# Kernel optimization log

Hardware: AMD Instinct MI355X
Metric: run time of the kernel (lower is better)

## Reference

```python
import jax, jax.numpy as jnp
import numpy as np
import math

IN_F, OUT_F = 4096, 4096
ORDER, TENSOR_RANK = 4, 8
LEAF_A = math.ceil(IN_F ** (1.0 / ORDER))   # 8
LEAF_B = math.ceil(OUT_F ** (1.0 / ORDER))  # 8


def setup_inputs() -> dict:
    key = jax.random.key(0)
    k1, k2, k3, k4 = jax.random.split(key, 4)
    x = jax.random.normal(k1, (8, 2048, IN_F), dtype=jnp.float32)
    weight = jax.random.normal(k2, (OUT_F, IN_F), dtype=jnp.float32) * 0.02
    bias = jax.random.normal(k3, (OUT_F,), dtype=jnp.float32) * 0.02
    # reset_parameters: gain for leaky_relu(sqrt(5)) = sqrt(2/(1+5)); std = gain / in_features**(1/order)
    gain = math.sqrt(2.0 / (1.0 + 5.0))
    std = gain / (IN_F ** (1.0 / ORDER))
    weight_leafs = jax.random.uniform(
        k4, (ORDER, TENSOR_RANK, LEAF_A, LEAF_B), dtype=jnp.float32,
        minval=-std, maxval=std)
    return {"x": x, "weight": weight, "bias": bias, "weight_leafs": weight_leafs}


def _reproduce_weight(weight_leafs):
    # Original einsum 'lij,rmn->rimjn' sums the FIRST operand over its leading
    # (rank) axis; chained through both stages + final .sum(0), every leaf is
    # summed over tensor_rank. Exact math = nested Kronecker of the rank-summed
    # leaves, sliced to [:in_features, :out_features].
    s = weight_leafs.sum(axis=1)  # (4, a, b)
    a, b = LEAF_A, LEAF_B
    z1 = jnp.einsum('ij,mn->imjn', s[0], s[1]).reshape(a * a, b * b)
    z2 = jnp.einsum('ij,mn->imjn', s[2], s[3]).reshape(a * a, b * b)
    zzz = jnp.einsum('ij,mn->imjn', z1, z2).reshape(a ** 4, b ** 4)
    return zzz[:IN_F, :OUT_F]  # (in_features, out_features)


def reference(x, weight, bias, weight_leafs):
    tensor_weight = _reproduce_weight(weight_leafs)       # (in, out)
    full_weight = weight + tensor_weight.T                # (out, in)
    # F.linear: x @ W^T + b
    return jnp.einsum('bsi,oi->bso', x, full_weight) + bias
```

## Files before the change

kernel.cpp:

```cpp
#include <hip/hip_runtime.h>
#include <hip/hip_bf16.h>
#include <stdint.h>

typedef __attribute__((ext_vector_type(8))) __bf16 bf16x8;
typedef __attribute__((ext_vector_type(4))) float f32x4;

#define IN_F   4096
#define OUT_F  4096
#define M_ROWS 16384

static __device__ __forceinline__ unsigned short f2bf(float f) {
    unsigned int u = __float_as_uint(f);
    u += 0x7FFFu + ((u >> 16) & 1u);
    return (unsigned short)(u >> 16);
}

#define PREP_WBLK 1366
#define PREP_NBLK 4096

__global__ __launch_bounds__(256) void prep_kernel(
    const float* __restrict__ weight, const float* __restrict__ leafs,
    const float* __restrict__ x,
    unsigned short* __restrict__ wb, unsigned short* __restrict__ xbuf)
{
    const int t = threadIdx.x;
    if (blockIdx.x < PREP_WBLK) {
        __shared__ float s[4][8][8];
        {
            const int o = t >> 6, a = (t >> 3) & 7, b = t & 7;
            float acc = 0.f;
            #pragma unroll
            for (int r = 0; r < 8; ++r)
                acc += leafs[o * 512 + r * 64 + a * 8 + b];
            s[o][a][b] = acc;
        }
        __syncthreads();

        const int total = (OUT_F * IN_F) / 8;
        for (int idx = blockIdx.x * 256 + t; idx < total; idx += PREP_WBLK * 256) {
            const int n  = idx >> 9;
            const int kg = idx & 511;
            const int n0 = n >> 9, n1 = (n >> 6) & 7, n2 = (n >> 3) & 7, n3 = n & 7;
            const int k0 = kg >> 6, k1 = (kg >> 3) & 7, k2 = kg & 7;
            const float p = s[0][k0][n0] * s[1][k1][n1] * s[2][k2][n2];
            const float4* wp = (const float4*)(weight + (size_t)n * IN_F + kg * 8);
            const float4 w0 = wp[0], w1 = wp[1];
            const float wv[8] = {w0.x, w0.y, w0.z, w0.w, w1.x, w1.y, w1.z, w1.w};
            unsigned int pk[4];
            #pragma unroll
            for (int j = 0; j < 4; ++j) {
                unsigned int lo = f2bf(wv[2*j]   + p * s[3][2*j]  [n3]);
                unsigned int hi = f2bf(wv[2*j+1] + p * s[3][2*j+1][n3]);
                pk[j] = lo | (hi << 16);
            }
            *reinterpret_cast<uint4*>(wb + (size_t)n * IN_F + kg * 8) =
                make_uint4(pk[0], pk[1], pk[2], pk[3]);
        }
    } else {
        const long long n8 = (long long)M_ROWS * IN_F / 8;
        const int xblocks = PREP_NBLK - PREP_WBLK;
        for (long long idx = (long long)(blockIdx.x - PREP_WBLK) * 256 + t;
             idx < n8; idx += (long long)xblocks * 256) {
            const float4* xp = (const float4*)(x + idx * 8);
            const float4 a = xp[0], b = xp[1];
            const float v[8] = {a.x, a.y, a.z, a.w, b.x, b.y, b.z, b.w};
            unsigned int pk[4];
            #pragma unroll
            for (int j = 0; j < 4; ++j)
                pk[j] = (unsigned int)f2bf(v[2*j]) | ((unsigned int)f2bf(v[2*j+1]) << 16);
            *reinterpret_cast<uint4*>(xbuf + idx * 8) =
                make_uint4(pk[0], pk[1], pk[2], pk[3]);
        }
    }
}

#define BK 64
#define NT 64

#define PANEL_A(b,kk) (ldsb + ((b)*2+(kk))*16384)
#define PANEL_B(b,kk) (ldsb + 65536 + ((b)*2+(kk))*16384)

#define GLL(src, dst) __builtin_amdgcn_global_load_lds( \
    (const __attribute__((address_space(1))) void*)(src), \
    (__attribute__((address_space(3))) void*)(dst), 16, 0, 0)

#define STAGE_A(b, kk, ko) do { \
    GLL(sA1 + (ko) + (kk)*32,          PANEL_A(b,kk) + d1); \
    GLL(sA1 + 524288 + (ko) + (kk)*32, PANEL_A(b,kk) + d1 + 8192); } while(0)
#define STAGE_B(b, kk, ko) do { \
    GLL(sB1 + (ko) + (kk)*32,          PANEL_B(b,kk) + d1); \
    GLL(sB1 + 524288 + (ko) + (kk)*32, PANEL_B(b,kk) + d1 + 8192); } while(0)

#define SB0  __builtin_amdgcn_sched_barrier(0)
#define BAR  __builtin_amdgcn_s_barrier()
#define PRI1 __builtin_amdgcn_s_setprio(1)
#define PRI0 __builtin_amdgcn_s_setprio(0)
#define WLG4 asm volatile("s_waitcnt lgkmcnt(4)" ::: "memory")
#define WLG0 asm volatile("s_waitcnt lgkmcnt(0)" ::: "memory")
#define WVM4 asm volatile("s_waitcnt vmcnt(4)" ::: "memory")
#define WVM0 asm volatile("s_waitcnt vmcnt(0)" ::: "memory")

#define HALF(P, KK, KO, PF) do { \
    if (PF) { STAGE_A((P)^1, KK, KO); STAGE_B((P)^1, KK, KO); } \
    _Pragma("unroll") \
    for (int i_ = 0; i_ < 4; ++i_) \
        aG1[i_] = *(const bf16x8*)(aB + (P)*32768 + (KK)*16384 + i_*1024); \
    _Pragma("unroll") \
    for (int i_ = 0; i_ < 4; ++i_) \
        bG[i_]  = *(const bf16x8*)(bB + (P)*32768 + (KK)*16384 + i_*1024); \
    _Pragma("unroll") \
    for (int i_ = 0; i_ < 4; ++i_) \
        aG2[i_] = *(const bf16x8*)(aB + (P)*32768 + (KK)*16384 + (4+i_)*1024); \
    SB0; WLG4; SB0; \
    PRI1; \
    _Pragma("unroll") \
    for (int m_ = 0; m_ < 4; ++m_) { _Pragma("unroll") \
    for (int n_ = 0; n_ < 4; ++n_) \
        acc[m_][n_] = __builtin_amdgcn_mfma_f32_16x16x32_bf16( \
            aG1[m_], bG[n_], acc[m_][n_], 0, 0, 0); } \
    PRI0; SB0; WLG0; SB0; \
    PRI1; \
    _Pragma("unroll") \
    for (int m_ = 0; m_ < 4; ++m_) { _Pragma("unroll") \
    for (int n_ = 0; n_ < 4; ++n_) \
        acc[4+m_][n_] = __builtin_amdgcn_mfma_f32_16x16x32_bf16( \
            aG2[m_], bG[n_], acc[4+m_][n_], 0, 0, 0); } \
    PRI0; SB0; \
    if (PF) { WVM4; } else { WVM0; } \
    BAR; SB0; \
} while (0)

__global__ __launch_bounds__(512, 2) void gemm2b_kernel(
    const unsigned short* __restrict__ xb,
    const unsigned short* __restrict__ wb,
    const float* __restrict__ bias,
    float* __restrict__ out)
{
    __shared__ unsigned short lds_us[65536];
    char* const ldsb = (char*)lds_us;

    const int t    = threadIdx.x;
    const int wave = t >> 6;
    const int lane = t & 63;
    const int lr   = lane & 15;
    const int kq   = lane >> 4;
    const int wr   = wave >> 2;
    const int wcn  = wave & 3;
    const int sx   = (lr & 6) << 3;

    const int bid  = blockIdx.x;
    const int swzb = (bid & 7) * 128 + (bid >> 3);
    const int bm   = (swzb >> 4) * 256;
    const int bn   = (swzb & 15) * 256;

    const int c1 = t;
    const int r1 = c1 >> 2;
    const int q1 = ((c1 & 3) * 16) ^ ((r1 & 6) << 3);
    const unsigned short* sA1 = xb + (size_t)(bm + r1) * IN_F + (q1 >> 1);
    const unsigned short* sB1 = wb + (size_t)(bn + r1) * IN_F + (q1 >> 1);
    const int d1 = c1 * 16;

    const char* aB = ldsb + (wr * 128 + lr) * 64 + ((kq * 16) ^ sx);
    const char* bB = ldsb + 65536 + (wcn * 64 + lr) * 64 + ((kq * 16) ^ sx);

    f32x4 acc[8][4] = {};
    bf16x8 aG1[4], aG2[4], bG[4];

    STAGE_A(0, 0, 0); STAGE_B(0, 0, 0); STAGE_A(0, 1, 0); STAGE_B(0, 1, 0);
    WVM4; BAR; SB0;

    #pragma unroll 1
    for (int tt = 0; tt < NT - 1; ++tt) {
        const int p  = tt & 1;
        const int ko = (tt + 1) * BK;
        HALF(p, 0, ko, true);
        HALF(p, 1, ko, true);
    }
    HALF(1, 0, 0, false);
    HALF(1, 1, 0, false);

    #pragma unroll
    for (int n = 0; n < 4; ++n) {
        const int col = bn + wcn * 64 + n * 16 + lr;
        const float bv = bias[col];
        #pragma unroll
        for (int m = 0; m < 8; ++m) {
            const size_t rb = (size_t)(bm + wr * 128 + m * 16 + kq * 4) * OUT_F + col;
            #pragma unroll
            for (int j = 0; j < 4; ++j)
                out[rb + (size_t)j * OUT_F] = acc[m][n][j] + bv;
        }
    }
}

#define FBM 128
#define FBN 128
#define FBK 32

__global__ __launch_bounds__(256) void gemm_fb_kernel(
    const float* __restrict__ xf,
    const unsigned short* __restrict__ wb,
    const float* __restrict__ bias,
    float* __restrict__ out)
{
    __shared__ unsigned short As[FBM * FBK];
    __shared__ unsigned short Bs[FBN * FBK];

    const int t    = threadIdx.x;
    const int wave = t >> 6;
    const int lane = t & 63;
    const int lr   = lane & 15;
    const int kq   = lane >> 4;
    const int wr   = wave >> 1;
    const int wc   = wave & 1;

    const int bm = blockIdx.x * FBM;
    const int bn = blockIdx.y * FBN;
    const int srow = t >> 2;
    const int scol = (t & 3) * 8;

    f32x4 acc[4][4] = {};

    for (int kt = 0; kt < IN_F; kt += FBK) {
        #pragma unroll
        for (int g = 0; g < 2; ++g) {
            const int row = srow + g * 64;
            const float4* xp = (const float4*)(xf + (size_t)(bm + row) * IN_F + kt + scol);
            const float4 a0 = xp[0], a1 = xp[1];
            const float v[8] = {a0.x, a0.y, a0.z, a0.w, a1.x, a1.y, a1.z, a1.w};
            unsigned int pk[4];
            #pragma unroll
            for (int j = 0; j < 4; ++j)
                pk[j] = (unsigned int)f2bf(v[2*j]) | ((unsigned int)f2bf(v[2*j+1]) << 16);
            *reinterpret_cast<uint4*>(&As[row * FBK + scol]) =
                make_uint4(pk[0], pk[1], pk[2], pk[3]);
        }
        {
            const unsigned short* gb0 = wb + (size_t)(bn + srow) * IN_F + kt + scol;
            const unsigned short* gb1 = gb0 + (size_t)64 * IN_F;
            GLL(gb0, Bs + srow * FBK + scol);
            GLL(gb1, Bs + (64 + srow) * FBK + scol);
        }
        __syncthreads();

        bf16x8 af[4], bfr[4];
        #pragma unroll
        for (int m = 0; m < 4; ++m)
            af[m] = *reinterpret_cast<const bf16x8*>(As + (wr * 64 + m * 16 + lr) * FBK + kq * 8);
        #pragma unroll
        for (int n = 0; n < 4; ++n)
            bfr[n] = *reinterpret_cast<const bf16x8*>(Bs + (wc * 64 + n * 16 + lr) * FBK + kq * 8);

        #pragma unroll
        for (int m = 0; m < 4; ++m)
            #pragma unroll
            for (int n = 0; n < 4; ++n)
                acc[m][n] = __builtin_amdgcn_mfma_f32_16x16x32_bf16(af[m], bfr[n], acc[m][n], 0, 0, 0);

        __syncthreads();
    }

    const int crow0 = kq * 4;
    #pragma unroll
    for (int n = 0; n < 4; ++n) {
        const int col = bn + wc * 64 + n * 16 + lr;
        const float bv = bias[col];
        #pragma unroll
        for (int m = 0; m < 4; ++m) {
            const int rowb = bm + wr * 64 + m * 16 + crow0;
            #pragma unroll
            for (int j = 0; j < 4; ++j)
                out[(size_t)(rowb + j) * OUT_F + col] = acc[m][n][j] + bv;
        }
    }
}

extern "C" void kernel_launch(void* const* d_in, const int* in_sizes, int n_in,
                              void* d_out, int out_size, void* d_ws, size_t ws_size,
                              hipStream_t stream) {
    const float* x      = (const float*)d_in[0];
    const float* weight = (const float*)d_in[1];
    const float* bias   = (const float*)d_in[2];
    const float* leafs  = (const float*)d_in[3];
    float* out = (float*)d_out;

    unsigned short* wb = (unsigned short*)d_ws;
    unsigned short* xbuf = (unsigned short*)((char*)d_ws +
                           (size_t)OUT_F * IN_F * sizeof(unsigned short));

    const size_t need_full = (size_t)OUT_F * IN_F * 2 + (size_t)M_ROWS * IN_F * 2;
    const bool full = ws_size >= need_full;

    if (full) {
        prep_kernel<<<dim3(PREP_NBLK), dim3(256), 0, stream>>>(
            weight, leafs, x, wb, xbuf);
        gemm2b_kernel<<<dim3((M_ROWS / 256) * (OUT_F / 256)), dim3(512), 0, stream>>>(
            xbuf, wb, bias, out);
    } else {
        prep_kernel<<<dim3(PREP_WBLK), dim3(256), 0, stream>>>(
            weight, leafs, x, wb, xbuf);
        gemm_fb_kernel<<<dim3(M_ROWS / FBM, OUT_F / FBN), dim3(256), 0, stream>>>(
            x, wb, bias, out);
    }
}
```

Baseline: 587.7 us.

## Restructure GEMM main loop into four-phase schedule with staggered A/B prefetch

Replaces the two-half-per-tile loop with a four-phase tile body. Each phase loads a subset of A/B fragments from LDS, issues global-to-LDS prefetch of the next A or B panel partway through, and runs a block of MFMAs between barriers. The goal is to interleave LDS reads, global loads and MFMA issue more finely, in the style of HipKittens-like 8-wave ping-pong schedules. It adds several more block barriers per tile and full vmcnt(0) waits, which could stall the pipeline.

```diff
diff --git a/kernel.cpp b/kernel.cpp
--- a/kernel.cpp
+++ b/kernel.cpp
@@ -95,42 +95,70 @@
 #define BAR  __builtin_amdgcn_s_barrier()
 #define PRI1 __builtin_amdgcn_s_setprio(1)
 #define PRI0 __builtin_amdgcn_s_setprio(0)
-#define WLG4 asm volatile("s_waitcnt lgkmcnt(4)" ::: "memory")
+#define WLG8 asm volatile("s_waitcnt lgkmcnt(8)" ::: "memory")
 #define WLG0 asm volatile("s_waitcnt lgkmcnt(0)" ::: "memory")
-#define WVM4 asm volatile("s_waitcnt vmcnt(4)" ::: "memory")
 #define WVM0 asm volatile("s_waitcnt vmcnt(0)" ::: "memory")
 
-#define HALF(P, KK, KO, PF) do { \
-    if (PF) { STAGE_A((P)^1, KK, KO); STAGE_B((P)^1, KK, KO); } \
-    _Pragma("unroll") \
-    for (int i_ = 0; i_ < 4; ++i_) \
-        aG1[i_] = *(const bf16x8*)(aB + (P)*32768 + (KK)*16384 + i_*1024); \
-    _Pragma("unroll") \
-    for (int i_ = 0; i_ < 4; ++i_) \
-        bG[i_]  = *(const bf16x8*)(bB + (P)*32768 + (KK)*16384 + i_*1024); \
-    _Pragma("unroll") \
-    for (int i_ = 0; i_ < 4; ++i_) \
-        aG2[i_] = *(const bf16x8*)(aB + (P)*32768 + (KK)*16384 + (4+i_)*1024); \
-    SB0; WLG4; SB0; \
-    PRI1; \
+#define MFMA16(a_, b_, c_) \
+    c_ = __builtin_amdgcn_mfma_f32_16x16x32_bf16(a_, b_, c_, 0, 0, 0)
+
+#define TILE(P, KO, PF) do { \
+     \
+    _Pragma("unroll") \
+    for (int m_ = 0; m_ < 4; ++m_) { _Pragma("unroll") \
+    for (int k_ = 0; k_ < 2; ++k_) \
+        aS1[m_][k_] = *(const bf16x8*)(aB + (P)*32768 + k_*16384 + m_*1024); } \
+    _Pragma("unroll") \
+    for (int n_ = 0; n_ < 2; ++n_) { _Pragma("unroll") \
+    for (int k_ = 0; k_ < 2; ++k_) \
+        bS[n_][k_] = *(const bf16x8*)(bB + (P)*32768 + k_*16384 + n_*1024); } \
+    SB0; WLG8; SB0; \
+    if (PF) { STAGE_A((P)^1, 0, KO); STAGE_A((P)^1, 1, KO); } \
+    BAR; WLG0; SB0; PRI1; \
+    _Pragma("unroll") \
+    for (int k_ = 0; k_ < 2; ++k_) { _Pragma("unroll") \
+    for (int m_ = 0; m_ < 4; ++m_) { _Pragma("unroll") \
+    for (int n_ = 0; n_ < 2; ++n_) \
+        MFMA16(aS1[m_][k_], bS[n_][k_], acc[m_][n_]); } } \
+    PRI0; BAR; \
+     \
+    _Pragma("unroll") \
+    for (int n_ = 0; n_ < 2; ++n_) { _Pragma("unroll") \
+    for (int k_ = 0; k_ < 2; ++k_) \
+        bS[2+n_][k_] = *(const bf16x8*)(bB + (P)*32768 + k_*16384 + (2+n_)*1024); } \
+    if (PF) { STAGE_B((P)^1, 0, KO); STAGE_B((P)^1, 1, KO); } \
+    BAR; WLG0; SB0; PRI1; \
+    _Pragma("unroll") \
+    for (int k_ = 0; k_ < 2; ++k_) { _Pragma("unroll") \
+    for (int m_ = 0; m_ < 4; ++m_) { _Pragma("unroll") \
+    for (int n_ = 0; n_ < 2; ++n_) \
+        MFMA16(aS1[m_][k_], bS[2+n_][k_], acc[m_][2+n_]); } } \
+    PRI0; BAR; \
+     \
+    _Pragma("unroll") \
+    for (int m_ = 0; m_ < 4; ++m_) \
+        aS2[m_][0] = *(const bf16x8*)(aB + (P)*32768 + (4+m_)*1024); \
+    BAR; WLG0; SB0; PRI1; \
     _Pragma("unroll") \
     for (int m_ = 0; m_ < 4; ++m_) { _Pragma("unroll") \
     for (int n_ = 0; n_ < 4; ++n_) \
-        acc[m_][n_] = __builtin_amdgcn_mfma_f32_16x16x32_bf16( \
-            aG1[m_], bG[n_], acc[m_][n_], 0, 0, 0); } \
-    PRI0; SB0; WLG0; SB0; \
-    PRI1; \
+        MFMA16(aS2[m_][0], bS[n_][0], acc[4+m_][n_]); } \
+    PRI0; BAR; \
+     \
+    _Pragma("unroll") \
+    for (int m_ = 0; m_ < 4; ++m_) \
+        aS2[m_][1] = *(const bf16x8*)(aB + (P)*32768 + 16384 + (4+m_)*1024); \
+    BAR; WLG0; SB0; PRI1; \
     _Pragma("unroll") \
     for (int m_ = 0; m_ < 4; ++m_) { _Pragma("unroll") \
     for (int n_ = 0; n_ < 4; ++n_) \
-        acc[4+m_][n_] = __builtin_amdgcn_mfma_f32_16x16x32_bf16( \
-            aG2[m_], bG[n_], acc[4+m_][n_], 0, 0, 0); } \
+        MFMA16(aS2[m_][1], bS[n_][1], acc[4+m_][n_]); } \
     PRI0; SB0; \
-    if (PF) { WVM4; } else { WVM0; } \
-    BAR; SB0; \
+    if (PF) { WVM0; } \
+    BAR; \
 } while (0)
 
-__global__ __launch_bounds__(512, 2) void gemm2b_kernel(
+__global__ __launch_bounds__(512, 2) void gemm4p_kernel(
     const unsigned short* __restrict__ xb,
     const unsigned short* __restrict__ wb,
     const float* __restrict__ bias,
@@ -164,20 +192,18 @@
     const char* bB = ldsb + 65536 + (wcn * 64 + lr) * 64 + ((kq * 16) ^ sx);
 
     f32x4 acc[8][4] = {};
-    bf16x8 aG1[4], aG2[4], bG[4];
-
-    STAGE_A(0, 0, 0); STAGE_B(0, 0, 0); STAGE_A(0, 1, 0); STAGE_B(0, 1, 0);
-    WVM4; BAR; SB0;
+    bf16x8 aS1[4][2], aS2[4][2], bS[4][2];
+
+    STAGE_A(0, 0, 0); STAGE_A(0, 1, 0); STAGE_B(0, 0, 0); STAGE_B(0, 1, 0);
+    WVM0; BAR;
 
     #pragma unroll 1
-    for (int tt = 0; tt < NT - 1; ++tt) {
-        const int p  = tt & 1;
-        const int ko = (tt + 1) * BK;
-        HALF(p, 0, ko, true);
-        HALF(p, 1, ko, true);
-    }
-    HALF(1, 0, 0, false);
-    HALF(1, 1, 0, false);
+    for (int tt = 0; tt < NT - 2; tt += 2) {
+        TILE(0, (tt + 1) * BK, true);
+        TILE(1, (tt + 2) * BK, true);
+    }
+    TILE(0, (NT - 1) * BK, true);
+    TILE(1, 0, false);
 
     #pragma unroll
     for (int n = 0; n < 4; ++n) {
@@ -294,7 +320,7 @@
     if (full) {
         prep_kernel<<<dim3(PREP_NBLK), dim3(256), 0, stream>>>(
             weight, leafs, x, wb, xbuf);
-        gemm2b_kernel<<<dim3((M_ROWS / 256) * (OUT_F / 256)), dim3(512), 0, stream>>>(
+        gemm4p_kernel<<<dim3((M_ROWS / 256) * (OUT_F / 256)), dim3(512), 0, stream>>>(
             xbuf, wb, bias, out);
     } else {
         prep_kernel<<<dim3(PREP_WBLK), dim3(256), 0, stream>>>(
```

Result: slower. 631.9 us (+7.5%).

## Load A operand directly from global into registers, stage only B in LDS

Applied to the files above, without the earlier changes.

The GEMM kernel stops staging the activation (A) tiles through LDS. Each wave now loads its A fragments straight from global memory into registers, double-buffered in aC/aN, while only the weight (B) tiles still go through LDS via global_load_lds. This halves LDS usage and LDS read traffic, and the vmcnt waits are reorganised to match. The cost is more register pressure, A reads that are not shared across the waves in a column, and global-load latency that now sits directly on the MFMA path.

```diff
diff --git a/kernel.cpp b/kernel.cpp
--- a/kernel.cpp
+++ b/kernel.cpp
@@ -77,16 +77,12 @@
 #define BK 64
 #define NT 64
 
-#define PANEL_A(b,kk) (ldsb + ((b)*2+(kk))*16384)
-#define PANEL_B(b,kk) (ldsb + 65536 + ((b)*2+(kk))*16384)
+#define PANEL_B(b,kk) (ldsb + ((b)*2+(kk))*16384)
 
 #define GLL(src, dst) __builtin_amdgcn_global_load_lds( \
     (const __attribute__((address_space(1))) void*)(src), \
     (__attribute__((address_space(3))) void*)(dst), 16, 0, 0)
 
-#define STAGE_A(b, kk, ko) do { \
-    GLL(sA1 + (ko) + (kk)*32,          PANEL_A(b,kk) + d1); \
-    GLL(sA1 + 524288 + (ko) + (kk)*32, PANEL_A(b,kk) + d1 + 8192); } while(0)
 #define STAGE_B(b, kk, ko) do { \
     GLL(sB1 + (ko) + (kk)*32,          PANEL_B(b,kk) + d1); \
     GLL(sB1 + 524288 + (ko) + (kk)*32, PANEL_B(b,kk) + d1 + 8192); } while(0)
@@ -95,48 +91,52 @@
 #define BAR  __builtin_amdgcn_s_barrier()
 #define PRI1 __builtin_amdgcn_s_setprio(1)
 #define PRI0 __builtin_amdgcn_s_setprio(0)
-#define WLG4 asm volatile("s_waitcnt lgkmcnt(4)" ::: "memory")
-#define WLG0 asm volatile("s_waitcnt lgkmcnt(0)" ::: "memory")
-#define WVM4 asm volatile("s_waitcnt vmcnt(4)" ::: "memory")
-#define WVM0 asm volatile("s_waitcnt vmcnt(0)" ::: "memory")
-
-#define HALF(P, KK, KO, PF) do { \
-    if (PF) { STAGE_A((P)^1, KK, KO); STAGE_B((P)^1, KK, KO); } \
-    _Pragma("unroll") \
-    for (int i_ = 0; i_ < 4; ++i_) \
-        aG1[i_] = *(const bf16x8*)(aB + (P)*32768 + (KK)*16384 + i_*1024); \
-    _Pragma("unroll") \
-    for (int i_ = 0; i_ < 4; ++i_) \
-        bG[i_]  = *(const bf16x8*)(bB + (P)*32768 + (KK)*16384 + i_*1024); \
-    _Pragma("unroll") \
-    for (int i_ = 0; i_ < 4; ++i_) \
-        aG2[i_] = *(const bf16x8*)(aB + (P)*32768 + (KK)*16384 + (4+i_)*1024); \
-    SB0; WLG4; SB0; \
-    PRI1; \
-    _Pragma("unroll") \
-    for (int m_ = 0; m_ < 4; ++m_) { _Pragma("unroll") \
+#define WLG0  asm volatile("s_waitcnt lgkmcnt(0)" ::: "memory")
+#define WVM12 asm volatile("s_waitcnt vmcnt(12)" ::: "memory")
+#define WVM8  asm volatile("s_waitcnt vmcnt(8)" ::: "memory")
+#define WVM0  asm volatile("s_waitcnt vmcnt(0)" ::: "memory")
+
+#define LDA8(dst, OFS) do { _Pragma("unroll") \
+    for (int m_ = 0; m_ < 8; ++m_) \
+        dst[m_] = *(const bf16x8*)(xbh + (OFS) + aoff[m_]); } while (0)
+
+#define LDB4(P, KK) do { _Pragma("unroll") \
+    for (int n_ = 0; n_ < 4; ++n_) \
+        bS[n_] = *(const bf16x8*)(bB + (P)*32768 + (KK)*16384 + n_*1024); } while (0)
+
+#define MM32(AS) do { _Pragma("unroll") \
+    for (int m_ = 0; m_ < 8; ++m_) { _Pragma("unroll") \
     for (int n_ = 0; n_ < 4; ++n_) \
         acc[m_][n_] = __builtin_amdgcn_mfma_f32_16x16x32_bf16( \
-            aG1[m_], bG[n_], acc[m_][n_], 0, 0, 0); } \
-    PRI0; SB0; WLG0; SB0; \
-    PRI1; \
-    _Pragma("unroll") \
-    for (int m_ = 0; m_ < 4; ++m_) { _Pragma("unroll") \
-    for (int n_ = 0; n_ < 4; ++n_) \
-        acc[4+m_][n_] = __builtin_amdgcn_mfma_f32_16x16x32_bf16( \
-            aG2[m_], bG[n_], acc[4+m_][n_], 0, 0, 0); } \
-    PRI0; SB0; \
-    if (PF) { WVM4; } else { WVM0; } \
+            AS[m_], bS[n_], acc[m_][n_], 0, 0, 0); } } while (0)
+
+#define TILEF(P, KO, PF) do { \
+    if (PF) { STAGE_B((P)^1, 0, KO); STAGE_B((P)^1, 1, KO); } \
+    LDA8(aN, 32); \
+    SB0; \
+    LDB4(P, 0); \
+    SB0; \
+    if (PF) { WVM12; } else { WVM8; } \
+    WLG0; SB0; \
+    PRI1; MM32(aC); PRI0; SB0; \
+    if (PF) LDA8(aC, 64); \
+    SB0; \
+    LDB4(P, 1); \
+    SB0; \
+    if (PF) { WVM8; } else { WVM0; } \
+    WLG0; SB0; \
+    PRI1; MM32(aN); PRI0; SB0; \
     BAR; SB0; \
+    xbh += 64; \
 } while (0)
 
-__global__ __launch_bounds__(512, 2) void gemm2b_kernel(
+__global__ __launch_bounds__(512, 2) void gemm_ad_kernel(
     const unsigned short* __restrict__ xb,
     const unsigned short* __restrict__ wb,
     const float* __restrict__ bias,
     float* __restrict__ out)
 {
-    __shared__ unsigned short lds_us[65536];
+    __shared__ unsigned short lds_us[32768];
     char* const ldsb = (char*)lds_us;
 
     const int t    = threadIdx.x;
@@ -153,31 +153,33 @@
     const int bm   = (swzb >> 4) * 256;
     const int bn   = (swzb & 15) * 256;
 
-    const int c1 = t;
-    const int r1 = c1 >> 2;
-    const int q1 = ((c1 & 3) * 16) ^ ((r1 & 6) << 3);
-    const unsigned short* sA1 = xb + (size_t)(bm + r1) * IN_F + (q1 >> 1);
+    const int r1 = t >> 2;
+    const int q1 = ((t & 3) * 16) ^ ((r1 & 6) << 3);
     const unsigned short* sB1 = wb + (size_t)(bn + r1) * IN_F + (q1 >> 1);
-    const int d1 = c1 * 16;
-
-    const char* aB = ldsb + (wr * 128 + lr) * 64 + ((kq * 16) ^ sx);
-    const char* bB = ldsb + 65536 + (wcn * 64 + lr) * 64 + ((kq * 16) ^ sx);
+    const int d1 = t * 16;
+
+    const char* bB = ldsb + (wcn * 64 + lr) * 64 + ((kq * 16) ^ sx);
+
+    const unsigned short* xbh = xb;
+    int aoff[8];
+    #pragma unroll
+    for (int m = 0; m < 8; ++m)
+        aoff[m] = (bm + wr * 128 + m * 16 + lr) * IN_F + kq * 8;
 
     f32x4 acc[8][4] = {};
-    bf16x8 aG1[4], aG2[4], bG[4];
-
-    STAGE_A(0, 0, 0); STAGE_B(0, 0, 0); STAGE_A(0, 1, 0); STAGE_B(0, 1, 0);
-    WVM4; BAR; SB0;
+    bf16x8 aC[8], aN[8], bS[4];
+
+    STAGE_B(0, 0, 0); STAGE_B(0, 1, 0);
+    LDA8(aC, 0);
+    SB0; WVM8; BAR; SB0;
 
     #pragma unroll 1
-    for (int tt = 0; tt < NT - 1; ++tt) {
-        const int p  = tt & 1;
-        const int ko = (tt + 1) * BK;
-        HALF(p, 0, ko, true);
-        HALF(p, 1, ko, true);
-    }
-    HALF(1, 0, 0, false);
-    HALF(1, 1, 0, false);
+    for (int tt = 0; tt < NT - 2; tt += 2) {
+        TILEF(0, (tt + 1) * BK, true);
+        TILEF(1, (tt + 2) * BK, true);
+    }
+    TILEF(0, (NT - 1) * BK, true);
+    TILEF(1, 0, false);
 
     #pragma unroll
     for (int n = 0; n < 4; ++n) {
@@ -294,7 +296,7 @@
     if (full) {
         prep_kernel<<<dim3(PREP_NBLK), dim3(256), 0, stream>>>(
             weight, leafs, x, wb, xbuf);
-        gemm2b_kernel<<<dim3((M_ROWS / 256) * (OUT_F / 256)), dim3(512), 0, stream>>>(
+        gemm_ad_kernel<<<dim3((M_ROWS / 256) * (OUT_F / 256)), dim3(512), 0, stream>>>(
             xbuf, wb, bias, out);
     } else {
         prep_kernel<<<dim3(PREP_WBLK), dim3(256), 0, stream>>>(
```

New measurement: 1.269 ms. 116% more time.
